# Performance work log

Hardware: AMD Instinct MI355X
Metric: run time of the kernel (lower is better)

The kernel has to match this reference:

```python
import jax, jax.numpy as jnp
import numpy as np

N_NODES = 100000
N_EDGES = 1600000
IN_C = 128
HID = 128
N_TRUCKS = 32


def _graph_conv(x, src, dst, W_rel, b_rel, W_root):
    # PyG GraphConv: out_i = lin_rel(sum_{j in N(i)} x_j) + lin_root(x_i)
    agg = jax.ops.segment_sum(x[src], dst, num_segments=N_NODES)  # [N, C_in]
    return agg @ W_rel + b_rel + x @ W_root


def setup_inputs() -> dict:
    key = jax.random.key(0)
    ks = jax.random.split(key, 12)
    s_in = 1.0 / np.sqrt(IN_C)
    s_h = 1.0 / np.sqrt(HID)
    x = jax.random.normal(ks[0], (N_NODES, IN_C), dtype=jnp.float32)
    edge_index = jax.random.randint(ks[1], (2, N_EDGES), 0, N_NODES, dtype=jnp.int32)
    inp = {"x": x, "edge_index": edge_index}
    # conv layer 0: in -> hid
    inp["W_rel0"] = jax.random.normal(ks[2], (IN_C, HID), jnp.float32) * s_in
    inp["b_rel0"] = jnp.zeros((HID,), jnp.float32)
    inp["W_root0"] = jax.random.normal(ks[3], (IN_C, HID), jnp.float32) * s_in
    # conv layers 1, 2: hid -> hid
    inp["W_rel1"] = jax.random.normal(ks[4], (HID, HID), jnp.float32) * s_h
    inp["b_rel1"] = jnp.zeros((HID,), jnp.float32)
    inp["W_root1"] = jax.random.normal(ks[5], (HID, HID), jnp.float32) * s_h
    inp["W_rel2"] = jax.random.normal(ks[6], (HID, HID), jnp.float32) * s_h
    inp["b_rel2"] = jnp.zeros((HID,), jnp.float32)
    inp["W_root2"] = jax.random.normal(ks[7], (HID, HID), jnp.float32) * s_h
    # edge classifier: Linear(hid,hid) -> ReLU -> Linear(hid,n_trucks)
    inp["Wc0"] = jax.random.normal(ks[8], (HID, HID), jnp.float32) * s_h
    inp["bc0"] = jnp.zeros((HID,), jnp.float32)
    inp["Wc1"] = jax.random.normal(ks[9], (HID, N_TRUCKS), jnp.float32) * s_h
    inp["bc1"] = jnp.zeros((N_TRUCKS,), jnp.float32)
    return inp


def reference(x, edge_index, W_rel0, b_rel0, W_root0, W_rel1, b_rel1, W_root1,
              W_rel2, b_rel2, W_root2, Wc0, bc0, Wc1, bc1):
    src, dst = edge_index[0], edge_index[1]
    h = jax.nn.relu(_graph_conv(x, src, dst, W_rel0, b_rel0, W_root0))
    h = jax.nn.relu(_graph_conv(h, src, dst, W_rel1, b_rel1, W_root1))
    h = jax.nn.relu(_graph_conv(h, src, dst, W_rel2, b_rel2, W_root2))
    # dropout = identity in eval mode
    h = jax.nn.relu(h @ Wc0 + bc0)
    logits = h @ Wc1 + bc1  # [N, num_trucks]
    return logits
```

## Files before the change

kernel.cpp:

```cpp
#include <hip/hip_runtime.h>
#include <cstdint>

#define N_NODES 100000
#define N_EDGES 1600000
#define HID 128
#define NT 32

#define BSHIFT 7
#define NB 782
#define NBLK_B 512
#define EPB 3328
#define ITER_B 13
#define CAP 2560

typedef __attribute__((ext_vector_type(8))) short short8v;
typedef __attribute__((ext_vector_type(4))) float f32x4;
typedef __attribute__((ext_vector_type(4))) unsigned uint4v;

__device__ inline unsigned short f2bf(float f) {
    union { float f; unsigned u; } v; v.f = f;
    unsigned r = v.u + 0x7FFF + ((v.u >> 16) & 1);
    return (unsigned short)(r >> 16);
}
__device__ inline float bf2f(unsigned short u) {
    union { unsigned u; float f; } v; v.u = ((unsigned)u) << 16; return v.f;
}
__device__ inline float bflo(unsigned v) { return bf2f((unsigned short)(v & 0xFFFF)); }
__device__ inline float bfhi(unsigned v) { return bf2f((unsigned short)(v >> 16)); }

__global__ __launch_bounds__(256) void k_bscatter2(const int* __restrict__ src,
                                                   const int* __restrict__ dst,
                                                   int* __restrict__ gcur,
                                                   unsigned* __restrict__ staged, int n) {
    __shared__ int lh[NB];
    __shared__ int lbase[NB];
    const int t = threadIdx.x;
    for (int i = t; i < NB; i += 256) lh[i] = 0;
    __syncthreads();
    const int base = blockIdx.x * EPB;
    #pragma unroll 1
    for (int i = 0; i < ITER_B; ++i) {
        int e = base + i * 256 + t;
        if (e < n) atomicAdd(&lh[dst[e] >> BSHIFT], 1);
    }
    __syncthreads();
    for (int i = t; i < NB; i += 256) {
        int c = lh[i];
        lbase[i] = c ? atomicAdd(&gcur[i], c) : 0;
        lh[i] = 0;
    }
    __syncthreads();
    #pragma unroll 1
    for (int i = 0; i < ITER_B; ++i) {
        int e = base + i * 256 + t;
        if (e < n) {
            int d = dst[e];
            int b = d >> BSHIFT;
            int pos = lbase[b] + atomicAdd(&lh[b], 1);
            if (pos < CAP)
                staged[(size_t)b * CAP + pos] = (unsigned)src[e] | ((unsigned)(d & 127) << 17);
        }
    }
}

__global__ __launch_bounds__(256) void k_bgroup2(const unsigned* __restrict__ staged,
                                                 const int* __restrict__ gcur,
                                                 int* __restrict__ offsets,
                                                 int* __restrict__ deg,
                                                 int* __restrict__ csr) {
    __shared__ int lh[128];
    __shared__ int lex[128];
    const int t = threadIdx.x;
    const int b = blockIdx.x;
    const int s0 = b * CAP;
    int cnt = gcur[b];
    if (cnt > CAP) cnt = CAP;
    if (t < 128) lh[t] = 0;
    __syncthreads();
    for (int i = t; i < cnt; i += 256)
        atomicAdd(&lh[staged[(size_t)s0 + i] >> 17], 1);
    __syncthreads();
    int myc = (t < 128) ? lh[t] : 0;
    if (t < 128) lex[t] = myc;
    __syncthreads();
    #pragma unroll 1
    for (int d = 1; d < 128; d <<= 1) {
        int add = 0;
        if (t < 128 && t >= d) add = lex[t - d];
        __syncthreads();
        if (t < 128) lex[t] += add;
        __syncthreads();
    }
    if (t < 128) {
        int excl = lex[t] - myc;
        lex[t] = excl;
        int node = (b << BSHIFT) + t;
        if (node < N_NODES) {
            offsets[node] = s0 + excl;
            deg[node] = myc;
        }
        lh[t] = 0;
    }
    __syncthreads();
    for (int i = t; i < cnt; i += 256) {
        unsigned v = staged[(size_t)s0 + i];
        int local = v >> 17;
        int p = s0 + lex[local] + atomicAdd(&lh[local], 1);
        csr[p] = (int)(v & 0x1FFFF);
    }
}

__global__ void k_cast(const float* __restrict__ in, unsigned short* __restrict__ out, int n8) {
    int i = blockIdx.x * 256 + threadIdx.x;
    if (i >= n8) return;
    const float4* p = reinterpret_cast<const float4*>(in + (size_t)i * 8);
    float4 a = p[0], b = p[1];
    union { unsigned short u[8]; uint4v v; } o;
    o.u[0] = f2bf(a.x); o.u[1] = f2bf(a.y); o.u[2] = f2bf(a.z); o.u[3] = f2bf(a.w);
    o.u[4] = f2bf(b.x); o.u[5] = f2bf(b.y); o.u[6] = f2bf(b.z); o.u[7] = f2bf(b.w);
    *reinterpret_cast<uint4v*>(out + (size_t)i * 8) = o.v;
}

struct WPrepArgs {
    const float* src[7];
    unsigned short* dst[7];
    int Ndim[7];
};

__global__ void k_prep_w(WPrepArgs a) {
    int m = blockIdx.x;
    const float* s = a.src[m];
    unsigned short* d = a.dst[m];
    int N = a.Ndim[m];
    int total = 128 * N;
    for (int idx = threadIdx.x; idx < total; idx += 256) {
        int n = idx >> 7;
        int k = idx & 127;
        d[n * 128 + k] = f2bf(s[(size_t)k * N + n]);
    }
}

__global__ __launch_bounds__(256) void k_agg_w(const unsigned short* __restrict__ X,
                                               const int* __restrict__ offsets,
                                               const int* __restrict__ deg,
                                               const int* __restrict__ csr,
                                               unsigned short* __restrict__ agg, int n) {
    int node = blockIdx.x * 4 + (threadIdx.x >> 6);
    if (node >= n) return;
    const int lane = threadIdx.x & 63;
    const int q = lane >> 4;
    const int c = lane & 15;
    const int e0 = offsets[node];
    const int e1 = e0 + deg[node];

    float s[8];
    #pragma unroll
    for (int j = 0; j < 8; ++j) s[j] = 0.f;

    int e = e0 + q;
    for (; e + 4 < e1; e += 8) {
        int i0 = csr[e];
        int i1 = csr[e + 4];
        uint4v v0 = *reinterpret_cast<const uint4v*>(X + (size_t)i0 * 128 + c * 8);
        uint4v v1 = *reinterpret_cast<const uint4v*>(X + (size_t)i1 * 128 + c * 8);
        #pragma unroll
        for (int j = 0; j < 4; ++j) {
            s[2 * j]     += bflo(v0[j]) + bflo(v1[j]);
            s[2 * j + 1] += bfhi(v0[j]) + bfhi(v1[j]);
        }
    }
    if (e < e1) {
        int i0 = csr[e];
        uint4v v0 = *reinterpret_cast<const uint4v*>(X + (size_t)i0 * 128 + c * 8);
        #pragma unroll
        for (int j = 0; j < 4; ++j) {
            s[2 * j]     += bflo(v0[j]);
            s[2 * j + 1] += bfhi(v0[j]);
        }
    }
    #pragma unroll
    for (int m = 16; m < 64; m <<= 1) {
        #pragma unroll
        for (int j = 0; j < 8; ++j) s[j] += __shfl_xor(s[j], m, 64);
    }
    if (q == 0) {
        union { unsigned short u[8]; uint4v v; } o;
        #pragma unroll
        for (int j = 0; j < 8; ++j) o.u[j] = f2bf(s[j]);
        *reinterpret_cast<uint4v*>(agg + (size_t)node * 128 + c * 8) = o.v;
    }
}

__global__ __launch_bounds__(256) void k_mfma128(
    const unsigned short* __restrict__ Xa, const unsigned short* __restrict__ WtA,
    const unsigned short* __restrict__ Xb, const unsigned short* __restrict__ WtB,
    const float* __restrict__ bias, unsigned short* __restrict__ Out,
    int M, int doRelu)
{
    __shared__ unsigned short wlds[128 * 136];

    const int t = threadIdx.x;
    const int lane = t & 63;
    const int w = t >> 6;
    const int r0 = blockIdx.x * 128;
    const int lrow = lane & 15;
    const int kg = lane >> 4;

    f32x4 acc[2][8];
    #pragma unroll
    for (int i = 0; i < 2; ++i)
        #pragma unroll
        for (int f = 0; f < 8; ++f) acc[i][f] = (f32x4){0.f, 0.f, 0.f, 0.f};

    #pragma unroll 1
    for (int sidx = 0; sidx < 2; ++sidx) {
        const unsigned short* X  = sidx ? Xb : Xa;
        const unsigned short* Wt = sidx ? WtB : WtA;
        if (!X) break;
        __syncthreads();
        {
            int n = t >> 1;
            int half = (t & 1) * 64;
            const unsigned short* srcp = Wt + (size_t)n * 128 + half;
            unsigned short* dstp = &wlds[n * 136 + half];
            #pragma unroll
            for (int j = 0; j < 8; ++j)
                *reinterpret_cast<uint4v*>(dstp + j * 8) =
                    *reinterpret_cast<const uint4v*>(srcp + j * 8);
        }
        __syncthreads();
        #pragma unroll 1
        for (int kc = 0; kc < 4; ++kc) {
            const int kb = kc * 32 + kg * 8;
            short8v a0 = {0,0,0,0,0,0,0,0}, a1 = {0,0,0,0,0,0,0,0};
            int row0 = r0 + w * 32 + lrow;
            int row1 = row0 + 16;
            if (row0 < M) a0 = *reinterpret_cast<const short8v*>(X + (size_t)row0 * 128 + kb);
            if (row1 < M) a1 = *reinterpret_cast<const short8v*>(X + (size_t)row1 * 128 + kb);
            #pragma unroll
            for (int f = 0; f < 8; ++f) {
                short8v b = *reinterpret_cast<const short8v*>(&wlds[(f * 16 + lrow) * 136 + kb]);
                acc[0][f] = __builtin_amdgcn_mfma_f32_16x16x32_bf16(a0, b, acc[0][f], 0, 0, 0);
                acc[1][f] = __builtin_amdgcn_mfma_f32_16x16x32_bf16(a1, b, acc[1][f], 0, 0, 0);
            }
        }
    }
    #pragma unroll
    for (int rr = 0; rr < 2; ++rr) {
        #pragma unroll
        for (int f = 0; f < 8; ++f) {
            int col = f * 16 + lrow;
            float bv = bias[col];
            #pragma unroll
            for (int reg = 0; reg < 4; ++reg) {
                int row = r0 + w * 32 + rr * 16 + kg * 4 + reg;
                if (row < M) {
                    float v = acc[rr][f][reg] + bv;
                    if (doRelu) v = fmaxf(v, 0.f);
                    Out[(size_t)row * 128 + col] = f2bf(v);
                }
            }
        }
    }
}

__global__ __launch_bounds__(256) void k_mfma32(
    const unsigned short* __restrict__ X, const unsigned short* __restrict__ Wt,
    const float* __restrict__ bias, float* __restrict__ Out, int M)
{
    __shared__ unsigned short wlds[32 * 136];

    const int t = threadIdx.x;
    const int lane = t & 63;
    const int w = t >> 6;
    const int r0 = blockIdx.x * 128;
    const int lrow = lane & 15;
    const int kg = lane >> 4;

    {
        int n = t >> 3;
        int seg = (t & 7) * 16;
        *reinterpret_cast<uint4v*>(&wlds[n * 136 + seg]) =
            *reinterpret_cast<const uint4v*>(Wt + (size_t)n * 128 + seg);
        *reinterpret_cast<uint4v*>(&wlds[n * 136 + seg + 8]) =
            *reinterpret_cast<const uint4v*>(Wt + (size_t)n * 128 + seg + 8);
    }
    __syncthreads();

    f32x4 acc[2][2];
    #pragma unroll
    for (int i = 0; i < 2; ++i)
        #pragma unroll
        for (int f = 0; f < 2; ++f) acc[i][f] = (f32x4){0.f, 0.f, 0.f, 0.f};

    #pragma unroll 1
    for (int kc = 0; kc < 4; ++kc) {
        const int kb = kc * 32 + kg * 8;
        short8v a0 = {0,0,0,0,0,0,0,0}, a1 = {0,0,0,0,0,0,0,0};
        int row0 = r0 + w * 32 + lrow;
        int row1 = row0 + 16;
        if (row0 < M) a0 = *reinterpret_cast<const short8v*>(X + (size_t)row0 * 128 + kb);
        if (row1 < M) a1 = *reinterpret_cast<const short8v*>(X + (size_t)row1 * 128 + kb);
        #pragma unroll
        for (int f = 0; f < 2; ++f) {
            short8v b = *reinterpret_cast<const short8v*>(&wlds[(f * 16 + lrow) * 136 + kb]);
            acc[0][f] = __builtin_amdgcn_mfma_f32_16x16x32_bf16(a0, b, acc[0][f], 0, 0, 0);
            acc[1][f] = __builtin_amdgcn_mfma_f32_16x16x32_bf16(a1, b, acc[1][f], 0, 0, 0);
        }
    }
    #pragma unroll
    for (int rr = 0; rr < 2; ++rr) {
        #pragma unroll
        for (int f = 0; f < 2; ++f) {
            int col = f * 16 + lrow;
            float bv = bias[col];
            #pragma unroll
            for (int reg = 0; reg < 4; ++reg) {
                int row = r0 + w * 32 + rr * 16 + kg * 4 + reg;
                if (row < M) Out[(size_t)row * 32 + col] = acc[rr][f][reg] + bv;
            }
        }
    }
}

extern "C" void kernel_launch(void* const* d_in, const int* in_sizes, int n_in,
                              void* d_out, int out_size, void* d_ws, size_t ws_size,
                              hipStream_t stream) {
    (void)in_sizes; (void)n_in; (void)out_size; (void)ws_size;

    const float* x      = (const float*)d_in[0];
    const int*   ei     = (const int*)d_in[1];
    const float* Wrel0  = (const float*)d_in[2];
    const float* brel0  = (const float*)d_in[3];
    const float* Wroot0 = (const float*)d_in[4];
    const float* Wrel1  = (const float*)d_in[5];
    const float* brel1  = (const float*)d_in[6];
    const float* Wroot1 = (const float*)d_in[7];
    const float* Wrel2  = (const float*)d_in[8];
    const float* brel2  = (const float*)d_in[9];
    const float* Wroot2 = (const float*)d_in[10];
    const float* Wc0    = (const float*)d_in[11];
    const float* bc0    = (const float*)d_in[12];
    const float* Wc1    = (const float*)d_in[13];
    const float* bc1    = (const float*)d_in[14];

    const int* src = ei;
    const int* dst = ei + N_EDGES;

    char* w = (char*)d_ws;
    auto alloc = [&](size_t bytes) {
        char* p = w;
        w += (bytes + 255) & ~(size_t)255;
        return (void*)p;
    };
    int* gcur    = (int*)alloc((size_t)NB * 4);
    int* offsets = (int*)alloc((size_t)N_NODES * 4);
    int* deg     = (int*)alloc((size_t)N_NODES * 4);
    unsigned* staged = (unsigned*)alloc((size_t)NB * CAP * 4);
    int* csr     = (int*)alloc((size_t)NB * CAP * 4);
    unsigned short* x_bf   = (unsigned short*)alloc((size_t)N_NODES * HID * 2);
    unsigned short* agg_bf = (unsigned short*)alloc((size_t)N_NODES * HID * 2);
    unsigned short* hA     = (unsigned short*)alloc((size_t)N_NODES * HID * 2);
    unsigned short* hB     = (unsigned short*)alloc((size_t)N_NODES * HID * 2);
    unsigned short* wtRel0  = (unsigned short*)alloc(128 * 128 * 2);
    unsigned short* wtRoot0 = (unsigned short*)alloc(128 * 128 * 2);
    unsigned short* wtRel1  = (unsigned short*)alloc(128 * 128 * 2);
    unsigned short* wtRoot1 = (unsigned short*)alloc(128 * 128 * 2);
    unsigned short* wtRel2  = (unsigned short*)alloc(128 * 128 * 2);
    unsigned short* wtRoot2 = (unsigned short*)alloc(128 * 128 * 2);
    unsigned short* wtC0    = (unsigned short*)alloc(128 * 128 * 2);
    unsigned short* wtC1    = (unsigned short*)alloc(32 * 128 * 2);

    (void)hipMemsetAsync(gcur, 0, (size_t)NB * 4, stream);
    k_bscatter2<<<NBLK_B, 256, 0, stream>>>(src, dst, gcur, staged, N_EDGES);
    k_bgroup2<<<NB, 256, 0, stream>>>(staged, gcur, offsets, deg, csr);

    k_cast<<<(N_NODES * HID / 8 + 255) / 256, 256, 0, stream>>>(x, x_bf, N_NODES * HID / 8);
    {
        WPrepArgs a;
        a.src[0] = Wrel0;  a.dst[0] = wtRel0;  a.Ndim[0] = 128;
        a.src[1] = Wroot0; a.dst[1] = wtRoot0; a.Ndim[1] = 128;
        a.src[2] = Wrel1;  a.dst[2] = wtRel1;  a.Ndim[2] = 128;
        a.src[3] = Wroot1; a.dst[3] = wtRoot1; a.Ndim[3] = 128;
        a.src[4] = Wrel2;  a.dst[4] = wtRel2;  a.Ndim[4] = 128;
        a.src[5] = Wroot2; a.dst[5] = wtRoot2; a.Ndim[5] = 128;
        a.src[6] = Wc0;    a.dst[6] = wtC0;    a.Ndim[6] = 128;
        k_prep_w<<<7, 256, 0, stream>>>(a);
        WPrepArgs b;
        b.src[0] = Wc1; b.dst[0] = wtC1; b.Ndim[0] = 32;
        for (int i = 1; i < 7; ++i) { b.src[i] = Wc1; b.dst[i] = wtC1; b.Ndim[i] = 32; }
        k_prep_w<<<1, 256, 0, stream>>>(b);
    }

    const int ab = (N_NODES + 3) / 4;
    const int gb = (N_NODES + 127) / 128;

    k_agg_w<<<ab, 256, 0, stream>>>(x_bf, offsets, deg, csr, agg_bf, N_NODES);
    k_mfma128<<<gb, 256, 0, stream>>>(agg_bf, wtRel0, x_bf, wtRoot0, brel0, hA, N_NODES, 1);
    k_agg_w<<<ab, 256, 0, stream>>>(hA, offsets, deg, csr, agg_bf, N_NODES);
    k_mfma128<<<gb, 256, 0, stream>>>(agg_bf, wtRel1, hA, wtRoot1, brel1, hB, N_NODES, 1);
    k_agg_w<<<ab, 256, 0, stream>>>(hB, offsets, deg, csr, agg_bf, N_NODES);
    k_mfma128<<<gb, 256, 0, stream>>>(agg_bf, wtRel2, hB, wtRoot2, brel2, hA, N_NODES, 1);
    k_mfma128<<<gb, 256, 0, stream>>>(hA, wtC0, nullptr, nullptr, bc0, hB, N_NODES, 1);
    k_mfma32<<<gb, 256, 0, stream>>>(hB, wtC1, bc1, (float*)d_out, N_NODES);
}
```

Measured before the change: 385.6 us.

## Fuse neighbor aggregation with GraphConv MFMA GEMM per 64-row tile

Replaces the separate aggregation kernel and GEMM kernel with one kernel per layer. Each block gathers neighbor sums for 64 nodes into LDS, then runs MFMA against the rel and root weights and writes the bias-ReLU output directly. This removes the round trip of the aggregated bf16 buffer through global memory and one launch per layer. In exchange, each wave processes 16 nodes serially with unroll 1, which may reduce memory-level parallelism in the latency-bound gather. The larger LDS footprint may also lower occupancy, and weights are reloaded per 64-row block instead of per 128-row block.

```diff
diff --git a/kernel.cpp b/kernel.cpp
--- a/kernel.cpp
+++ b/kernel.cpp
@@ -140,54 +140,139 @@
     }
 }
 
-__global__ __launch_bounds__(256) void k_agg_w(const unsigned short* __restrict__ X,
-                                               const int* __restrict__ offsets,
-                                               const int* __restrict__ deg,
-                                               const int* __restrict__ csr,
-                                               unsigned short* __restrict__ agg, int n) {
-    int node = blockIdx.x * 4 + (threadIdx.x >> 6);
-    if (node >= n) return;
-    const int lane = threadIdx.x & 63;
+__global__ __launch_bounds__(256) void k_fused(
+    const unsigned short* __restrict__ X,
+    const unsigned short* __restrict__ WtRel,
+    const unsigned short* __restrict__ WtRoot,
+    const float* __restrict__ bias,
+    const int* __restrict__ offsets, const int* __restrict__ deg,
+    const int* __restrict__ csr,
+    unsigned short* __restrict__ Out, int M)
+{
+    __shared__ unsigned short alds[64 * 136];
+    __shared__ unsigned short wlds[128 * 136];
+
+    const int t = threadIdx.x;
+    const int lane = t & 63;
+    const int w = t >> 6;
+    const int r0 = blockIdx.x * 64;
     const int q = lane >> 4;
     const int c = lane & 15;
-    const int e0 = offsets[node];
-    const int e1 = e0 + deg[node];
-
-    float s[8];
-    #pragma unroll
-    for (int j = 0; j < 8; ++j) s[j] = 0.f;
-
-    int e = e0 + q;
-    for (; e + 4 < e1; e += 8) {
-        int i0 = csr[e];
-        int i1 = csr[e + 4];
-        uint4v v0 = *reinterpret_cast<const uint4v*>(X + (size_t)i0 * 128 + c * 8);
-        uint4v v1 = *reinterpret_cast<const uint4v*>(X + (size_t)i1 * 128 + c * 8);
-        #pragma unroll
-        for (int j = 0; j < 4; ++j) {
-            s[2 * j]     += bflo(v0[j]) + bflo(v1[j]);
-            s[2 * j + 1] += bfhi(v0[j]) + bfhi(v1[j]);
-        }
-    }
-    if (e < e1) {
-        int i0 = csr[e];
-        uint4v v0 = *reinterpret_cast<const uint4v*>(X + (size_t)i0 * 128 + c * 8);
-        #pragma unroll
-        for (int j = 0; j < 4; ++j) {
-            s[2 * j]     += bflo(v0[j]);
-            s[2 * j + 1] += bfhi(v0[j]);
-        }
-    }
-    #pragma unroll
-    for (int m = 16; m < 64; m <<= 1) {
-        #pragma unroll
-        for (int j = 0; j < 8; ++j) s[j] += __shfl_xor(s[j], m, 64);
-    }
-    if (q == 0) {
-        union { unsigned short u[8]; uint4v v; } o;
-        #pragma unroll
-        for (int j = 0; j < 8; ++j) o.u[j] = f2bf(s[j]);
-        *reinterpret_cast<uint4v*>(agg + (size_t)node * 128 + c * 8) = o.v;
+
+    #pragma unroll 1
+    for (int i = 0; i < 16; ++i) {
+        const int row = w * 16 + i;
+        const int node = r0 + row;
+        float s[8];
+        #pragma unroll
+        for (int j = 0; j < 8; ++j) s[j] = 0.f;
+        if (node < M) {
+            const int e0 = offsets[node];
+            const int e1 = e0 + deg[node];
+            int e = e0 + q;
+            for (; e + 4 < e1; e += 8) {
+                int i0 = csr[e];
+                int i1 = csr[e + 4];
+                uint4v v0 = *reinterpret_cast<const uint4v*>(X + (size_t)i0 * 128 + c * 8);
+                uint4v v1 = *reinterpret_cast<const uint4v*>(X + (size_t)i1 * 128 + c * 8);
+                #pragma unroll
+                for (int j = 0; j < 4; ++j) {
+                    s[2 * j]     += bflo(v0[j]) + bflo(v1[j]);
+                    s[2 * j + 1] += bfhi(v0[j]) + bfhi(v1[j]);
+                }
+            }
+            if (e < e1) {
+                int i0 = csr[e];
+                uint4v v0 = *reinterpret_cast<const uint4v*>(X + (size_t)i0 * 128 + c * 8);
+                #pragma unroll
+                for (int j = 0; j < 4; ++j) {
+                    s[2 * j]     += bflo(v0[j]);
+                    s[2 * j + 1] += bfhi(v0[j]);
+                }
+            }
+        }
+        #pragma unroll
+        for (int m = 16; m < 64; m <<= 1) {
+            #pragma unroll
+            for (int j = 0; j < 8; ++j) s[j] += __shfl_xor(s[j], m, 64);
+        }
+        if (q == 0) {
+            union { unsigned short u[8]; uint4v v; } o;
+            #pragma unroll
+            for (int j = 0; j < 8; ++j) o.u[j] = f2bf(s[j]);
+            *reinterpret_cast<uint4v*>(&alds[row * 136 + c * 8]) = o.v;
+        }
+    }
+    __syncthreads();
+
+    {
+        int n = t >> 1;
+        int half = (t & 1) * 64;
+        const unsigned short* srcp = WtRel + (size_t)n * 128 + half;
+        unsigned short* dstp = &wlds[n * 136 + half];
+        #pragma unroll
+        for (int j = 0; j < 8; ++j)
+            *reinterpret_cast<uint4v*>(dstp + j * 8) =
+                *reinterpret_cast<const uint4v*>(srcp + j * 8);
+    }
+    __syncthreads();
+
+    f32x4 acc[8];
+    #pragma unroll
+    for (int f = 0; f < 8; ++f) acc[f] = (f32x4){0.f, 0.f, 0.f, 0.f};
+
+    #pragma unroll 1
+    for (int kc = 0; kc < 4; ++kc) {
+        const int kb = kc * 32 + q * 8;
+        short8v a = *reinterpret_cast<const short8v*>(&alds[(w * 16 + c) * 136 + kb]);
+        #pragma unroll
+        for (int f = 0; f < 8; ++f) {
+            short8v b = *reinterpret_cast<const short8v*>(&wlds[(f * 16 + c) * 136 + kb]);
+            acc[f] = __builtin_amdgcn_mfma_f32_16x16x32_bf16(a, b, acc[f], 0, 0, 0);
+        }
+    }
+    __syncthreads();
+
+    {
+        int n = t >> 1;
+        int half = (t & 1) * 64;
+        const unsigned short* srcp = WtRoot + (size_t)n * 128 + half;
+        unsigned short* dstp = &wlds[n * 136 + half];
+        #pragma unroll
+        for (int j = 0; j < 8; ++j)
+            *reinterpret_cast<uint4v*>(dstp + j * 8) =
+                *reinterpret_cast<const uint4v*>(srcp + j * 8);
+    }
+    __syncthreads();
+
+    {
+        const int row = r0 + w * 16 + c;
+        #pragma unroll 1
+        for (int kc = 0; kc < 4; ++kc) {
+            const int kb = kc * 32 + q * 8;
+            short8v a = {0,0,0,0,0,0,0,0};
+            if (row < M) a = *reinterpret_cast<const short8v*>(X + (size_t)row * 128 + kb);
+            #pragma unroll
+            for (int f = 0; f < 8; ++f) {
+                short8v b = *reinterpret_cast<const short8v*>(&wlds[(f * 16 + c) * 136 + kb]);
+                acc[f] = __builtin_amdgcn_mfma_f32_16x16x32_bf16(a, b, acc[f], 0, 0, 0);
+            }
+        }
+    }
+
+    #pragma unroll
+    for (int f = 0; f < 8; ++f) {
+        int col = f * 16 + c;
+        float bv = bias[col];
+        #pragma unroll
+        for (int reg = 0; reg < 4; ++reg) {
+            int row = r0 + w * 16 + q * 4 + reg;
+            if (row < M) {
+                float v = acc[f][reg] + bv;
+                v = fmaxf(v, 0.f);
+                Out[(size_t)row * 128 + col] = f2bf(v);
+            }
+        }
     }
 }
 
@@ -359,7 +444,6 @@
     unsigned* staged = (unsigned*)alloc((size_t)NB * CAP * 4);
     int* csr     = (int*)alloc((size_t)NB * CAP * 4);
     unsigned short* x_bf   = (unsigned short*)alloc((size_t)N_NODES * HID * 2);
-    unsigned short* agg_bf = (unsigned short*)alloc((size_t)N_NODES * HID * 2);
     unsigned short* hA     = (unsigned short*)alloc((size_t)N_NODES * HID * 2);
     unsigned short* hB     = (unsigned short*)alloc((size_t)N_NODES * HID * 2);
     unsigned short* wtRel0  = (unsigned short*)alloc(128 * 128 * 2);
@@ -392,15 +476,12 @@
         k_prep_w<<<1, 256, 0, stream>>>(b);
     }
 
-    const int ab = (N_NODES + 3) / 4;
+    const int fb = (N_NODES + 63) / 64;
     const int gb = (N_NODES + 127) / 128;
 
-    k_agg_w<<<ab, 256, 0, stream>>>(x_bf, offsets, deg, csr, agg_bf, N_NODES);
-    k_mfma128<<<gb, 256, 0, stream>>>(agg_bf, wtRel0, x_bf, wtRoot0, brel0, hA, N_NODES, 1);
-    k_agg_w<<<ab, 256, 0, stream>>>(hA, offsets, deg, csr, agg_bf, N_NODES);
-    k_mfma128<<<gb, 256, 0, stream>>>(agg_bf, wtRel1, hA, wtRoot1, brel1, hB, N_NODES, 1);
-    k_agg_w<<<ab, 256, 0, stream>>>(hB, offsets, deg, csr, agg_bf, N_NODES);
-    k_mfma128<<<gb, 256, 0, stream>>>(agg_bf, wtRel2, hB, wtRoot2, brel2, hA, N_NODES, 1);
+    k_fused<<<fb, 256, 0, stream>>>(x_bf, wtRel0, wtRoot0, brel0, offsets, deg, csr, hA, N_NODES);
+    k_fused<<<fb, 256, 0, stream>>>(hA,   wtRel1, wtRoot1, brel1, offsets, deg, csr, hB, N_NODES);
+    k_fused<<<fb, 256, 0, stream>>>(hB,   wtRel2, wtRoot2, brel2, offsets, deg, csr, hA, N_NODES);
     k_mfma128<<<gb, 256, 0, stream>>>(hA, wtC0, nullptr, nullptr, bc0, hB, N_NODES, 1);
     k_mfma32<<<gb, 256, 0, stream>>>(hB, wtC1, bc1, (float*)d_out, N_NODES);
 }
```

New measurement: 564.2 us. +46.3%, slower.

## Fuse last graph conv and classifier MLP into one tail kernel; unroll gather

Applied to the files above, without the earlier changes.

The third conv's dense transform, the first classifier layer and the final 32-wide projection are merged into one kernel. Intermediate 128-row tiles stay in LDS instead of round-tripping through global memory, and two launches disappear. The aggregation loop also processes four neighbors per iteration instead of two to raise memory-level parallelism. The fused kernel uses about 70KB of LDS per block, which limits occupancy.

```diff
diff --git a/kernel.cpp b/kernel.cpp
--- a/kernel.cpp
+++ b/kernel.cpp
@@ -158,18 +158,22 @@
     for (int j = 0; j < 8; ++j) s[j] = 0.f;
 
     int e = e0 + q;
-    for (; e + 4 < e1; e += 8) {
+    for (; e + 12 < e1; e += 16) {
         int i0 = csr[e];
         int i1 = csr[e + 4];
+        int i2 = csr[e + 8];
+        int i3 = csr[e + 12];
         uint4v v0 = *reinterpret_cast<const uint4v*>(X + (size_t)i0 * 128 + c * 8);
         uint4v v1 = *reinterpret_cast<const uint4v*>(X + (size_t)i1 * 128 + c * 8);
+        uint4v v2 = *reinterpret_cast<const uint4v*>(X + (size_t)i2 * 128 + c * 8);
+        uint4v v3 = *reinterpret_cast<const uint4v*>(X + (size_t)i3 * 128 + c * 8);
         #pragma unroll
         for (int j = 0; j < 4; ++j) {
-            s[2 * j]     += bflo(v0[j]) + bflo(v1[j]);
-            s[2 * j + 1] += bfhi(v0[j]) + bfhi(v1[j]);
-        }
-    }
-    if (e < e1) {
+            s[2 * j]     += (bflo(v0[j]) + bflo(v1[j])) + (bflo(v2[j]) + bflo(v3[j]));
+            s[2 * j + 1] += (bfhi(v0[j]) + bfhi(v1[j])) + (bfhi(v2[j]) + bfhi(v3[j]));
+        }
+    }
+    for (; e < e1; e += 4) {
         int i0 = csr[e];
         uint4v v0 = *reinterpret_cast<const uint4v*>(X + (size_t)i0 * 128 + c * 8);
         #pragma unroll
@@ -264,11 +268,16 @@
     }
 }
 
-__global__ __launch_bounds__(256) void k_mfma32(
-    const unsigned short* __restrict__ X, const unsigned short* __restrict__ Wt,
-    const float* __restrict__ bias, float* __restrict__ Out, int M)
+__global__ __launch_bounds__(256) void k_tail(
+    const unsigned short* __restrict__ Xa, const unsigned short* __restrict__ WtA,
+    const unsigned short* __restrict__ Xb, const unsigned short* __restrict__ WtB,
+    const float* __restrict__ bias,
+    const unsigned short* __restrict__ WtC0, const float* __restrict__ bc0,
+    const unsigned short* __restrict__ WtC1, const float* __restrict__ bc1,
+    float* __restrict__ Out, int M)
 {
-    __shared__ unsigned short wlds[32 * 136];
+    __shared__ unsigned short alds[128 * 136];
+    __shared__ unsigned short wlds[128 * 136];
 
     const int t = threadIdx.x;
     const int lane = t & 63;
@@ -277,35 +286,127 @@
     const int lrow = lane & 15;
     const int kg = lane >> 4;
 
+    f32x4 acc[2][8];
+    #pragma unroll
+    for (int i = 0; i < 2; ++i)
+        #pragma unroll
+        for (int f = 0; f < 8; ++f) acc[i][f] = (f32x4){0.f, 0.f, 0.f, 0.f};
+
+    #pragma unroll 1
+    for (int sidx = 0; sidx < 2; ++sidx) {
+        const unsigned short* X  = sidx ? Xb : Xa;
+        const unsigned short* Wt = sidx ? WtB : WtA;
+        __syncthreads();
+        {
+            int n = t >> 1;
+            int half = (t & 1) * 64;
+            const unsigned short* srcp = Wt + (size_t)n * 128 + half;
+            unsigned short* dstp = &wlds[n * 136 + half];
+            #pragma unroll
+            for (int j = 0; j < 8; ++j)
+                *reinterpret_cast<uint4v*>(dstp + j * 8) =
+                    *reinterpret_cast<const uint4v*>(srcp + j * 8);
+        }
+        __syncthreads();
+        #pragma unroll 1
+        for (int kc = 0; kc < 4; ++kc) {
+            const int kb = kc * 32 + kg * 8;
+            short8v a0 = {0,0,0,0,0,0,0,0}, a1 = {0,0,0,0,0,0,0,0};
+            int row0 = r0 + w * 32 + lrow;
+            int row1 = row0 + 16;
+            if (row0 < M) a0 = *reinterpret_cast<const short8v*>(X + (size_t)row0 * 128 + kb);
+            if (row1 < M) a1 = *reinterpret_cast<const short8v*>(X + (size_t)row1 * 128 + kb);
+            #pragma unroll
+            for (int f = 0; f < 8; ++f) {
+                short8v b = *reinterpret_cast<const short8v*>(&wlds[(f * 16 + lrow) * 136 + kb]);
+                acc[0][f] = __builtin_amdgcn_mfma_f32_16x16x32_bf16(a0, b, acc[0][f], 0, 0, 0);
+                acc[1][f] = __builtin_amdgcn_mfma_f32_16x16x32_bf16(a1, b, acc[1][f], 0, 0, 0);
+            }
+        }
+    }
+    __syncthreads();
+    #pragma unroll
+    for (int rr = 0; rr < 2; ++rr) {
+        #pragma unroll
+        for (int f = 0; f < 8; ++f) {
+            int col = f * 16 + lrow;
+            float bv = bias[col];
+            #pragma unroll
+            for (int reg = 0; reg < 4; ++reg) {
+                int row = w * 32 + rr * 16 + kg * 4 + reg;
+                alds[row * 136 + col] = f2bf(fmaxf(acc[rr][f][reg] + bv, 0.f));
+            }
+        }
+    }
+    {
+        int n = t >> 1;
+        int half = (t & 1) * 64;
+        const unsigned short* srcp = WtC0 + (size_t)n * 128 + half;
+        unsigned short* dstp = &wlds[n * 136 + half];
+        #pragma unroll
+        for (int j = 0; j < 8; ++j)
+            *reinterpret_cast<uint4v*>(dstp + j * 8) =
+                *reinterpret_cast<const uint4v*>(srcp + j * 8);
+    }
+    __syncthreads();
+
+    f32x4 acc2[2][8];
+    #pragma unroll
+    for (int i = 0; i < 2; ++i)
+        #pragma unroll
+        for (int f = 0; f < 8; ++f) acc2[i][f] = (f32x4){0.f, 0.f, 0.f, 0.f};
+    #pragma unroll 1
+    for (int kc = 0; kc < 4; ++kc) {
+        const int kb = kc * 32 + kg * 8;
+        short8v a0 = *reinterpret_cast<const short8v*>(&alds[(w * 32 + lrow) * 136 + kb]);
+        short8v a1 = *reinterpret_cast<const short8v*>(&alds[(w * 32 + 16 + lrow) * 136 + kb]);
+        #pragma unroll
+        for (int f = 0; f < 8; ++f) {
+            short8v b = *reinterpret_cast<const short8v*>(&wlds[(f * 16 + lrow) * 136 + kb]);
+            acc2[0][f] = __builtin_amdgcn_mfma_f32_16x16x32_bf16(a0, b, acc2[0][f], 0, 0, 0);
+            acc2[1][f] = __builtin_amdgcn_mfma_f32_16x16x32_bf16(a1, b, acc2[1][f], 0, 0, 0);
+        }
+    }
+    __syncthreads();
+
+    #pragma unroll
+    for (int rr = 0; rr < 2; ++rr) {
+        #pragma unroll
+        for (int f = 0; f < 8; ++f) {
+            int col = f * 16 + lrow;
+            float bv = bc0[col];
+            #pragma unroll
+            for (int reg = 0; reg < 4; ++reg) {
+                int row = w * 32 + rr * 16 + kg * 4 + reg;
+                alds[row * 136 + col] = f2bf(fmaxf(acc2[rr][f][reg] + bv, 0.f));
+            }
+        }
+    }
     {
         int n = t >> 3;
         int seg = (t & 7) * 16;
         *reinterpret_cast<uint4v*>(&wlds[n * 136 + seg]) =
-            *reinterpret_cast<const uint4v*>(Wt + (size_t)n * 128 + seg);
+            *reinterpret_cast<const uint4v*>(WtC1 + (size_t)n * 128 + seg);
         *reinterpret_cast<uint4v*>(&wlds[n * 136 + seg + 8]) =
-            *reinterpret_cast<const uint4v*>(Wt + (size_t)n * 128 + seg + 8);
-    }
-    __syncthreads();
-
-    f32x4 acc[2][2];
+            *reinterpret_cast<const uint4v*>(WtC1 + (size_t)n * 128 + seg + 8);
+    }
+    __syncthreads();
+
+    f32x4 acc3[2][2];
     #pragma unroll
     for (int i = 0; i < 2; ++i)
         #pragma unroll
-        for (int f = 0; f < 2; ++f) acc[i][f] = (f32x4){0.f, 0.f, 0.f, 0.f};
-
+        for (int f = 0; f < 2; ++f) acc3[i][f] = (f32x4){0.f, 0.f, 0.f, 0.f};
     #pragma unroll 1
     for (int kc = 0; kc < 4; ++kc) {
         const int kb = kc * 32 + kg * 8;
-        short8v a0 = {0,0,0,0,0,0,0,0}, a1 = {0,0,0,0,0,0,0,0};
-        int row0 = r0 + w * 32 + lrow;
-        int row1 = row0 + 16;
-        if (row0 < M) a0 = *reinterpret_cast<const short8v*>(X + (size_t)row0 * 128 + kb);
-        if (row1 < M) a1 = *reinterpret_cast<const short8v*>(X + (size_t)row1 * 128 + kb);
+        short8v a0 = *reinterpret_cast<const short8v*>(&alds[(w * 32 + lrow) * 136 + kb]);
+        short8v a1 = *reinterpret_cast<const short8v*>(&alds[(w * 32 + 16 + lrow) * 136 + kb]);
         #pragma unroll
         for (int f = 0; f < 2; ++f) {
             short8v b = *reinterpret_cast<const short8v*>(&wlds[(f * 16 + lrow) * 136 + kb]);
-            acc[0][f] = __builtin_amdgcn_mfma_f32_16x16x32_bf16(a0, b, acc[0][f], 0, 0, 0);
-            acc[1][f] = __builtin_amdgcn_mfma_f32_16x16x32_bf16(a1, b, acc[1][f], 0, 0, 0);
+            acc3[0][f] = __builtin_amdgcn_mfma_f32_16x16x32_bf16(a0, b, acc3[0][f], 0, 0, 0);
+            acc3[1][f] = __builtin_amdgcn_mfma_f32_16x16x32_bf16(a1, b, acc3[1][f], 0, 0, 0);
         }
     }
     #pragma unroll
@@ -313,11 +414,11 @@
         #pragma unroll
         for (int f = 0; f < 2; ++f) {
             int col = f * 16 + lrow;
-            float bv = bias[col];
+            float bv = bc1[col];
             #pragma unroll
             for (int reg = 0; reg < 4; ++reg) {
                 int row = r0 + w * 32 + rr * 16 + kg * 4 + reg;
-                if (row < M) Out[(size_t)row * 32 + col] = acc[rr][f][reg] + bv;
+                if (row < M) Out[(size_t)row * 32 + col] = acc3[rr][f][reg] + bv;
             }
         }
     }
@@ -400,7 +501,6 @@
     k_agg_w<<<ab, 256, 0, stream>>>(hA, offsets, deg, csr, agg_bf, N_NODES);
     k_mfma128<<<gb, 256, 0, stream>>>(agg_bf, wtRel1, hA, wtRoot1, brel1, hB, N_NODES, 1);
     k_agg_w<<<ab, 256, 0, stream>>>(hB, offsets, deg, csr, agg_bf, N_NODES);
-    k_mfma128<<<gb, 256, 0, stream>>>(agg_bf, wtRel2, hB, wtRoot2, brel2, hA, N_NODES, 1);
-    k_mfma128<<<gb, 256, 0, stream>>>(hA, wtC0, nullptr, nullptr, bc0, hB, N_NODES, 1);
-    k_mfma32<<<gb, 256, 0, stream>>>(hB, wtC1, bc1, (float*)d_out, N_NODES);
-}
+    k_tail<<<gb, 256, 0, stream>>>(agg_bf, wtRel2, hB, wtRoot2, brel2,
+                                   wtC0, bc0, wtC1, bc1, (float*)d_out, N_NODES);
+}
```

Result: faster. 356.4 us (-7.6%).
